# Optimization experiments

Measured on AMD Instinct MI355X. Metric: run time of the kernel, lower is better.

## Reference

```python
import jax, jax.numpy as jnp
import numpy as np

VOCAB = 100000
EMB = 300
HID = 512            # bidirectional total; per-direction = 256
HD = HID // 2
TAGS = 12
START = 10
STOP = 11
NEG = -10000.0
T = 4096


def _lstm_dir(x, h0, c0, Wih, Whh, bih, bhh, reverse):
    # x: [T, EMB]; PyTorch gate order i, f, g, o
    def step(carry, xt):
        h, c = carry
        g = xt @ Wih.T + h @ Whh.T + bih + bhh           # [4*HD]
        i, f, gg, o = jnp.split(g, 4)
        i = jax.nn.sigmoid(i); f = jax.nn.sigmoid(f)
        gg = jnp.tanh(gg); o = jax.nn.sigmoid(o)
        c = f * c + i * gg
        h = o * jnp.tanh(c)
        return (h, c), h
    _, hs = jax.lax.scan(step, (h0, c0), x, reverse=reverse)
    return hs                                            # [T, HD]


def setup_inputs() -> dict:
    key = jax.random.key(0)
    ks = jax.random.split(key, 16)
    s = 0.05  # weight scale for numerical stability
    sentence = jax.random.randint(ks[0], (T,), 0, VOCAB)
    h0 = jax.random.normal(ks[1], (2, HD), jnp.float32)
    c0 = jax.random.normal(ks[2], (2, HD), jnp.float32)
    embed = jax.random.normal(ks[3], (VOCAB, EMB), jnp.float32) * s
    W_ih_f = jax.random.normal(ks[4], (4 * HD, EMB), jnp.float32) * s
    W_hh_f = jax.random.normal(ks[5], (4 * HD, HD), jnp.float32) * s
    b_ih_f = jax.random.normal(ks[6], (4 * HD,), jnp.float32) * s
    b_hh_f = jax.random.normal(ks[7], (4 * HD,), jnp.float32) * s
    W_ih_b = jax.random.normal(ks[8], (4 * HD, EMB), jnp.float32) * s
    W_hh_b = jax.random.normal(ks[9], (4 * HD, HD), jnp.float32) * s
    b_ih_b = jax.random.normal(ks[10], (4 * HD,), jnp.float32) * s
    b_hh_b = jax.random.normal(ks[11], (4 * HD,), jnp.float32) * s
    W_tag = jax.random.normal(ks[12], (TAGS, HID), jnp.float32) * s
    b_tag = jax.random.normal(ks[13], (TAGS,), jnp.float32) * s
    transitions = jax.random.normal(ks[14], (TAGS, TAGS), jnp.float32)
    transitions = transitions.at[START, :].set(NEG).at[:, STOP].set(NEG)
    return dict(sentence=sentence, h0=h0, c0=c0, embed=embed,
                W_ih_f=W_ih_f, W_hh_f=W_hh_f, b_ih_f=b_ih_f, b_hh_f=b_hh_f,
                W_ih_b=W_ih_b, W_hh_b=W_hh_b, b_ih_b=b_ih_b, b_hh_b=b_hh_b,
                W_tag=W_tag, b_tag=b_tag, transitions=transitions)


def reference(sentence, h0, c0, embed,
              W_ih_f, W_hh_f, b_ih_f, b_hh_f,
              W_ih_b, W_hh_b, b_ih_b, b_hh_b,
              W_tag, b_tag, transitions):
    # --- BiLSTM features (dropout layers are identity at inference) ---
    x = embed[sentence]                                      # [T, EMB]
    hf = _lstm_dir(x, h0[0], c0[0], W_ih_f, W_hh_f, b_ih_f, b_hh_f, False)
    hb = _lstm_dir(x, h0[1], c0[1], W_ih_b, W_hh_b, b_ih_b, b_hh_b, True)
    feats = jnp.concatenate([hf, hb], axis=-1) @ W_tag.T + b_tag  # [T, TAGS]

    # --- Viterbi decode: transitions[to, from] ---
    init = jnp.full((TAGS,), NEG, jnp.float32).at[START].set(0.0)

    def vstep(fv, feat):
        ntv = fv[None, :] + transitions                      # [to, from]
        bp = jnp.argmax(ntv, axis=1)                         # best prev tag per 'to'
        fv2 = jnp.max(ntv, axis=1) + feat
        return fv2, bp

    fv, bps = jax.lax.scan(vstep, init, feats)               # bps: [T, TAGS]
    terminal = fv + transitions[STOP]
    best = jnp.argmax(terminal)
    path_score = terminal[best]

    def back(tag, bp):
        return bp[tag], tag

    _, best_path = jax.lax.scan(back, best, bps, reverse=True)  # [T] tags in time order
    return path_score, best_path
```

## Files before the change

### kernel.cpp

```cpp
#include <hip/hip_runtime.h>

#define T_LEN 4096
#define EMB   300
#define HD    256
#define G4    1024
#define N2    2048
#define TAGS  12
#define NEGV  -10000.0f
#define SENT  0x7F7F7F7Fu
#define NLSTM 29

#define MV(K) { const float4 hv = h4[K];                    \
    a0 = fmaf(wA##K.x, hv.x, a0);                           \
    a1 = fmaf(wA##K.y, hv.y, a1);                           \
    a2 = fmaf(wA##K.z, hv.z, a2);                           \
    a3 = fmaf(wA##K.w, hv.w, a3); }

__global__ __launch_bounds__(1024) void fused_gemm_lstm(
    const int* __restrict__ sent, const float* __restrict__ embed,
    const float* __restrict__ Wihf, const float* __restrict__ Wihb,
    const float* __restrict__ bihf, const float* __restrict__ bhhf,
    const float* __restrict__ bihb, const float* __restrict__ bhhb,
    const float* Whh_f, const float* Whh_b,
    const float* __restrict__ h0, const float* __restrict__ c0,
    float* gin,
    float* Hh)
{
    __shared__ __align__(16) char smem[145*1024];
    const int blk = blockIdx.x;
    const int tid = threadIdx.x;

    if (blk >= NLSTM) {
        float* AsT  = (float*)smem;
        float* BsT  = (float*)(smem + 8704);
        int*   sIdx = (int*)  (smem + 17408);
        const int g  = blk - NLSTM;
        const int kk8 = g >> 5;
        const int bn  = g & 31;
        const int bm  = (kk8 & 1) ? (63 - (kk8 >> 1)) : (kk8 >> 1);

        if (tid < 64) sIdx[tid] = sent[bm*64 + tid];
        __syncthreads();

        const int srow = tid >> 4;
        const int skj  = (tid & 15) << 1;
        const int m0   = (tid >> 5) << 1;
        const int n0   = (tid & 31) << 1;
        const int rn   = bn * 64;
        float acc00=0.f, acc01=0.f, acc10=0.f, acc11=0.f;

        for (int kc = 0; kc < 10; ++kc) {
            const int k0 = kc*32 + skj;
            float2 va = make_float2(0.f, 0.f), vb = make_float2(0.f, 0.f);
            if (k0 + 1 < EMB) {
                va = *(const float2*)(embed + (long)sIdx[srow]*EMB + k0);
                const int r = rn + srow;
                const float* bsrc = (r < G4) ? (Wihf + (long)r*EMB)
                                             : (Wihb + (long)(r-G4)*EMB);
                vb = *(const float2*)(bsrc + k0);
            }
            AsT[skj*68 + srow]     = va.x;
            AsT[(skj+1)*68 + srow] = va.y;
            BsT[skj*68 + srow]     = vb.x;
            BsT[(skj+1)*68 + srow] = vb.y;
            __syncthreads();
            #pragma unroll
            for (int kk = 0; kk < 32; ++kk) {
                const float2 a2v = *(const float2*)&AsT[kk*68 + m0];
                const float2 b2v = *(const float2*)&BsT[kk*68 + n0];
                acc00 = fmaf(a2v.x, b2v.x, acc00);
                acc01 = fmaf(a2v.x, b2v.y, acc01);
                acc10 = fmaf(a2v.y, b2v.x, acc10);
                acc11 = fmaf(a2v.y, b2v.y, acc11);
            }
            __syncthreads();
        }

        const int c0i = rn + n0, c1i = c0i + 1;
        const float bias0 = (c0i < G4) ? (bihf[c0i] + bhhf[c0i])
                                       : (bihb[c0i-G4] + bhhb[c0i-G4]);
        const float bias1 = (c1i < G4) ? (bihf[c1i] + bhhf[c1i])
                                       : (bihb[c1i-G4] + bhhb[c1i-G4]);
        const long t0 = (long)(bm*64 + m0), t1 = t0 + 1;
        __hip_atomic_store(&gin[t0*N2 + c0i], acc00 + bias0,
                           __ATOMIC_RELAXED, __HIP_MEMORY_SCOPE_AGENT);
        __hip_atomic_store(&gin[t0*N2 + c1i], acc01 + bias1,
                           __ATOMIC_RELAXED, __HIP_MEMORY_SCOPE_AGENT);
        __hip_atomic_store(&gin[t1*N2 + c0i], acc10 + bias0,
                           __ATOMIC_RELAXED, __HIP_MEMORY_SCOPE_AGENT);
        __hip_atomic_store(&gin[t1*N2 + c1i], acc11 + bias1,
                           __ATOMIC_RELAXED, __HIP_MEMORY_SCOPE_AGENT);
        return;
    }

    const int m8 = blk & 7;
    if (m8 != 0 && m8 != 4) return;
    const int dir = (m8 == 4);
    const int b   = blk >> 3;
    const int u     = tid & 63;
    const int wvid  = tid >> 6;
    const int gate  = wvid >> 2;
    const int q     = wvid & 3;
    const int unit0 = b*64;
    const int row   = gate*64 + u;
    const int grow  = gate*HD + unit0 + u;

    float* hS  = (float*)smem;
    float* ps  = (float*)(smem + 1024);
    float* gvS = (float*)(smem + 4096);

    const float4* W4 = (const float4*)((dir ? Whh_b : Whh_f)
                                       + (long)grow*HD + q*64);
    const float4 wA0  = W4[0],  wA1  = W4[1],  wA2  = W4[2],  wA3  = W4[3];
    const float4 wA4  = W4[4],  wA5  = W4[5],  wA6  = W4[6],  wA7  = W4[7];
    const float4 wA8  = W4[8],  wA9  = W4[9],  wA10 = W4[10], wA11 = W4[11];
    const float4 wA12 = W4[12], wA13 = W4[13], wA14 = W4[14], wA15 = W4[15];

    float cst = 0.f;
    if (tid < 64) cst = c0[dir*HD + unit0 + tid];
    if (tid < HD) hS[tid] = h0[dir*HD + tid];

    float* ginD = gin + dir*G4;
    float gx;
    {
        const long gi0 = (long)(dir ? T_LEN-1 : 0)*N2 + grow;
        do {
            gx = __hip_atomic_load(&ginD[gi0], __ATOMIC_RELAXED,
                                   __HIP_MEMORY_SCOPE_AGENT);
        } while (__float_as_uint(gx) == SENT);
    }

    #pragma unroll 1
    for (int s = 0; s < T_LEN; ++s) {
        const int t = dir ? (T_LEN-1-s) : s;
        float gxn = 0.f;
        long  gidx = 0;
        if (s+1 < T_LEN) {
            gidx = (long)(dir ? t-1 : t+1)*N2 + grow;
            gxn = __hip_atomic_load(&ginD[gidx], __ATOMIC_RELAXED,
                                    __HIP_MEMORY_SCOPE_AGENT);
            __builtin_amdgcn_sched_barrier(0);
        }

        __syncthreads();
        const float4* h4 = (const float4*)(hS + q*64);
        float a0=0.f, a1=0.f, a2=0.f, a3=0.f;
        MV(0)  MV(1)  MV(2)  MV(3)
        MV(4)  MV(5)  MV(6)  MV(7)
        MV(8)  MV(9)  MV(10) MV(11)
        MV(12) MV(13) MV(14) MV(15)
        const float a = (a0+a1)+(a2+a3);
        if (q != 0) ps[(q-1)*256 + row] = a;
        __syncthreads();

        if (q == 0) {
            const float raw = a + ps[row] + ps[256+row] + ps[512+row] + gx;
            gvS[row] = (gate == 2) ? tanhf(raw) : 1.f/(1.f + expf(-raw));
        }
        __syncthreads();

        if (tid < 64) {
            const float i_ = gvS[tid],       f_ = gvS[64+tid];
            const float g_ = gvS[128+tid],   o_ = gvS[192+tid];
            cst = fmaf(f_, cst, i_*g_);
            const float hv = o_ * tanhf(cst);
            hS[unit0 + tid] = hv;
            __hip_atomic_store(&Hh[(long)t*512 + dir*HD + unit0 + tid], hv,
                               __ATOMIC_RELAXED, __HIP_MEMORY_SCOPE_AGENT);
        } else if (tid < 256 && s+1 < T_LEN) {
            const int fidx = tid - 64;
            const int gu   = (fidx < unit0) ? fidx : fidx + 64;
            const long idx = (long)t*512 + dir*HD + gu;
            float v;
            do {
                v = __hip_atomic_load(&Hh[idx], __ATOMIC_RELAXED,
                                      __HIP_MEMORY_SCOPE_AGENT);
            } while (__float_as_uint(v) == SENT);
            hS[gu] = v;
        }

        if (s+1 < T_LEN) {
            while (__float_as_uint(gxn) == SENT)
                gxn = __hip_atomic_load(&ginD[gidx], __ATOMIC_RELAXED,
                                        __HIP_MEMORY_SCOPE_AGENT);
        }
        gx = gxn;
    }
}

__global__ __launch_bounds__(192) void feats_kernel(
    const float* __restrict__ Hhist, const float* __restrict__ Wtag,
    const float* __restrict__ btag, float* __restrict__ feats)
{
    __shared__ __align__(16) float Ws[TAGS][512];
    const int tid = threadIdx.x;
    for (int i = tid; i < TAGS*512; i += 192) Ws[0][i] = Wtag[i];
    __syncthreads();
    const int tl = tid / TAGS;
    const int tg = tid % TAGS;
    const int t  = blockIdx.x * 16 + tl;
    const float4* hrow = (const float4*)(Hhist + (long)t*512);
    const float4* wrow = (const float4*)(&Ws[tg][0]);
    float a0=0.f,a1=0.f,a2=0.f,a3=0.f;
    #pragma unroll 8
    for (int k = 0; k < 128; ++k) {
        const float4 h = hrow[k];
        const float4 ww = wrow[k];
        a0=fmaf(h.x,ww.x,a0); a1=fmaf(h.y,ww.y,a1);
        a2=fmaf(h.z,ww.z,a2); a3=fmaf(h.w,ww.w,a3);
    }
    feats[t*TAGS + tg] = ((a0+a1)+(a2+a3)) + btag[tg];
}

__global__ __launch_bounds__(256) void viterbi_kernel(
    const float* __restrict__ feats, const float* __restrict__ trans,
    float* __restrict__ out)
{
    __shared__ float fS[256*TAGS];
    __shared__ unsigned char bps[T_LEN*TAGS];
    __shared__ float fvS[TAGS];
    const int tid = threadIdx.x;

    float tr[TAGS];
    float fv = NEGV;
    if (tid < TAGS) {
        #pragma unroll
        for (int f = 0; f < TAGS; ++f) tr[f] = trans[tid*TAGS + f];
        fv = (tid == 10) ? 0.f : NEGV;
    }

    for (int c = 0; c < T_LEN/256; ++c) {
        __syncthreads();
        for (int i = tid; i < 256*TAGS; i += 256) fS[i] = feats[c*256*TAGS + i];
        __syncthreads();
        if (tid < TAGS) {
            for (int s = 0; s < 256; ++s) {
                float best = -3.4e38f; int bp = 0;
                #pragma unroll
                for (int f = 0; f < TAGS; ++f) {
                    const float v = __shfl(fv, f, 64) + tr[f];
                    if (v > best) { best = v; bp = f; }
                }
                bps[(c*256+s)*TAGS + tid] = (unsigned char)bp;
                fv = best + fS[s*TAGS + tid];
            }
        }
    }
    __syncthreads();
    if (tid < TAGS) fvS[tid] = fv + trans[11*TAGS + tid];
    __syncthreads();
    if (tid == 0) {
        float bestv = fvS[0]; int best = 0;
        #pragma unroll
        for (int g = 1; g < TAGS; ++g) if (fvS[g] > bestv) { bestv = fvS[g]; best = g; }
        out[0] = bestv;
        int cur = best;
        for (int t = T_LEN-1; t >= 0; --t) {
            out[1+t] = (float)cur;
            cur = bps[t*TAGS + cur];
        }
    }
}

extern "C" void kernel_launch(void* const* d_in, const int* in_sizes, int n_in,
                              void* d_out, int out_size, void* d_ws, size_t ws_size,
                              hipStream_t stream)
{
    (void)in_sizes; (void)n_in; (void)out_size; (void)ws_size;
    const int*   sentence = (const int*)  d_in[0];
    const float* h0       = (const float*)d_in[1];
    const float* c0       = (const float*)d_in[2];
    const float* embed    = (const float*)d_in[3];
    const float* Wihf     = (const float*)d_in[4];
    const float* Whhf     = (const float*)d_in[5];
    const float* bihf     = (const float*)d_in[6];
    const float* bhhf     = (const float*)d_in[7];
    const float* Wihb     = (const float*)d_in[8];
    const float* Whhb     = (const float*)d_in[9];
    const float* bihb     = (const float*)d_in[10];
    const float* bhhb     = (const float*)d_in[11];
    const float* Wtag     = (const float*)d_in[12];
    const float* btag     = (const float*)d_in[13];
    const float* trans    = (const float*)d_in[14];
    float* out = (float*)d_out;

    float* gin   = (float*)d_ws;
    float* Hh    = gin + (long)T_LEN*N2;
    float* feats = Hh  + (long)T_LEN*512;

    hipMemsetAsync(gin, 0x7F, (size_t)T_LEN*N2*sizeof(float), stream);
    hipMemsetAsync(Hh,  0x7F, (size_t)T_LEN*512*sizeof(float), stream);

    fused_gemm_lstm<<<NLSTM + 2048, 1024, 0, stream>>>(
        sentence, embed, Wihf, Wihb, bihf, bhhf, bihb, bhhb,
        Whhf, Whhb, h0, c0, gin, Hh);
    feats_kernel<<<T_LEN/16, 192, 0, stream>>>(Hh, Wtag, btag, feats);
    viterbi_kernel<<<1, 256, 0, stream>>>(feats, trans, out);
}
```

Before: 7.332 ms.

## Split Viterbi into max-only serial recursion plus parallel backpointer pass

The serial Viterbi loop now computes only the max over the twelve predecessor scores with an fmax tree, storing each step's forward vector to workspace, instead of doing shuffle-based argmax with compares and branches. Backpointers are then recomputed in parallel afterwards by all 64 lanes from the stored forward vectors. The aim is to shorten the per-step dependency chain on the serial critical path. In exchange, each step now needs two block barriers and an LDS broadcast where the old version used register shuffles, and it adds global stores every step plus a recompute pass.

```diff
diff --git a/kernel.cpp b/kernel.cpp
--- a/kernel.cpp
+++ b/kernel.cpp
@@ -9,6 +9,7 @@
 #define NEGV  -10000.0f
 #define SENT  0x7F7F7F7Fu
 #define NLSTM 29
+#define VCH   512
 
 #define MV(K) { const float4 hv = h4[K];                    \
     a0 = fmaf(wA##K.x, hv.x, a0);                           \
@@ -212,47 +213,82 @@
     feats[t*TAGS + tg] = ((a0+a1)+(a2+a3)) + btag[tg];
 }
 
-__global__ __launch_bounds__(256) void viterbi_kernel(
+__global__ __launch_bounds__(64) void viterbi_kernel(
     const float* __restrict__ feats, const float* __restrict__ trans,
-    float* __restrict__ out)
+    float* __restrict__ fvstore, float* __restrict__ out)
 {
-    __shared__ float fS[256*TAGS];
+    __shared__ __align__(16) float fS[VCH*TAGS];
+    __shared__ __align__(16) float fvS[16];
+    __shared__ __align__(16) float trS[TAGS*TAGS];
     __shared__ unsigned char bps[T_LEN*TAGS];
-    __shared__ float fvS[TAGS];
-    const int tid = threadIdx.x;
-
+    const int lane = threadIdx.x;
+
+    for (int i = lane; i < TAGS*TAGS; i += 64) trS[i] = trans[i];
+
+    const int trow = (lane < TAGS) ? lane : 0;
     float tr[TAGS];
-    float fv = NEGV;
-    if (tid < TAGS) {
+    #pragma unroll
+    for (int f = 0; f < TAGS; ++f) tr[f] = trans[trow*TAGS + f];
+
+    float fvv[TAGS];
+    #pragma unroll
+    for (int f = 0; f < TAGS; ++f) fvv[f] = (f == 10) ? 0.f : NEGV;
+
+    for (int c = 0; c < T_LEN/VCH; ++c) {
+        __syncthreads();
+        {
+            const float4* src = (const float4*)(feats + (long)c*VCH*TAGS);
+            float4* dst = (float4*)fS;
+            #pragma unroll 4
+            for (int i = lane; i < VCH*TAGS/4; i += 64) dst[i] = src[i];
+        }
+        __syncthreads();
+        for (int s = 0; s < VCH; ++s) {
+            const int t = c*VCH + s;
+            if (lane < TAGS) {
+                fvstore[(long)t*TAGS + lane] = fvv[lane];
+                float cand[TAGS];
+                #pragma unroll
+                for (int f = 0; f < TAGS; ++f) cand[f] = fvv[f] + tr[f];
+                const float m =
+                    fmaxf(fmaxf(fmaxf(fmaxf(cand[0],cand[1]), fmaxf(cand[2],cand[3])),
+                                fmaxf(fmaxf(cand[4],cand[5]), fmaxf(cand[6],cand[7]))),
+                          fmaxf(fmaxf(cand[8],cand[9]), fmaxf(cand[10],cand[11])));
+                fvS[lane] = m + fS[s*TAGS + lane];
+            }
+            __syncthreads();
+            const float4 A = *(const float4*)&fvS[0];
+            const float4 B = *(const float4*)&fvS[4];
+            const float4 C = *(const float4*)&fvS[8];
+            fvv[0]=A.x; fvv[1]=A.y; fvv[2]=A.z; fvv[3]=A.w;
+            fvv[4]=B.x; fvv[5]=B.y; fvv[6]=B.z; fvv[7]=B.w;
+            fvv[8]=C.x; fvv[9]=C.y; fvv[10]=C.z; fvv[11]=C.w;
+            __syncthreads();
+        }
+    }
+
+    __syncthreads();
+    for (int idx = lane; idx < T_LEN*TAGS; idx += 64) {
+        const int t  = idx / TAGS;
+        const int to = idx - t*TAGS;
+        const float* fp = fvstore + (long)t*TAGS;
+        float best = -3.4e38f; int bp = 0;
         #pragma unroll
-        for (int f = 0; f < TAGS; ++f) tr[f] = trans[tid*TAGS + f];
-        fv = (tid == 10) ? 0.f : NEGV;
-    }
-
-    for (int c = 0; c < T_LEN/256; ++c) {
-        __syncthreads();
-        for (int i = tid; i < 256*TAGS; i += 256) fS[i] = feats[c*256*TAGS + i];
-        __syncthreads();
-        if (tid < TAGS) {
-            for (int s = 0; s < 256; ++s) {
-                float best = -3.4e38f; int bp = 0;
-                #pragma unroll
-                for (int f = 0; f < TAGS; ++f) {
-                    const float v = __shfl(fv, f, 64) + tr[f];
-                    if (v > best) { best = v; bp = f; }
-                }
-                bps[(c*256+s)*TAGS + tid] = (unsigned char)bp;
-                fv = best + fS[s*TAGS + tid];
-            }
-        }
+        for (int f = 0; f < TAGS; ++f) {
+            const float v = fp[f] + trS[to*TAGS + f];
+            if (v > best) { best = v; bp = f; }
+        }
+        bps[idx] = (unsigned char)bp;
     }
     __syncthreads();
-    if (tid < TAGS) fvS[tid] = fv + trans[11*TAGS + tid];
-    __syncthreads();
-    if (tid == 0) {
-        float bestv = fvS[0]; int best = 0;
+
+    if (lane == 0) {
+        float bestv = -3.4e38f; int best = 0;
         #pragma unroll
-        for (int g = 1; g < TAGS; ++g) if (fvS[g] > bestv) { bestv = fvS[g]; best = g; }
+        for (int g = 0; g < TAGS; ++g) {
+            const float v = fvv[g] + trS[11*TAGS + g];
+            if (v > bestv) { bestv = v; best = g; }
+        }
         out[0] = bestv;
         int cur = best;
         for (int t = T_LEN-1; t >= 0; --t) {
@@ -284,9 +320,10 @@
     const float* trans    = (const float*)d_in[14];
     float* out = (float*)d_out;
 
-    float* gin   = (float*)d_ws;
-    float* Hh    = gin + (long)T_LEN*N2;
-    float* feats = Hh  + (long)T_LEN*512;
+    float* gin     = (float*)d_ws;
+    float* Hh      = gin   + (long)T_LEN*N2;
+    float* feats   = Hh    + (long)T_LEN*512;
+    float* fvstore = feats + (long)T_LEN*TAGS;
 
     hipMemsetAsync(gin, 0x7F, (size_t)T_LEN*N2*sizeof(float), stream);
     hipMemsetAsync(Hh,  0x7F, (size_t)T_LEN*512*sizeof(float), stream);
@@ -295,5 +332,5 @@
         sentence, embed, Wihf, Wihb, bihf, bhhf, bihb, bhhb,
         Whhf, Whhb, h0, c0, gin, Hh);
     feats_kernel<<<T_LEN/16, 192, 0, stream>>>(Hh, Wtag, btag, feats);
-    viterbi_kernel<<<1, 256, 0, stream>>>(feats, trans, out);
+    viterbi_kernel<<<1, 64, 0, stream>>>(feats, trans, fvstore, out);
 }
```

Measured after the change: 6.815 ms. -7.1%, faster.
